# Performance work log

Measured on AMD Instinct MI355X. Metric: run time of the kernel, lower is better.

Reference implementation:

```python
import jax, jax.numpy as jnp
import numpy as np

N = 20000        # num_nodes
E = 320000       # num_edges
B = 2            # batch_size (query rows)
F = 64           # in_features == nrela_dim == out_features
R = 32           # num_relations
NEG_SLOPE = 0.2  # LeakyReLU alpha
RATIO = 0.5      # fixed ratio (ratio-given branch of forward)
ITERS = 4
LN_EPS = 1e-5


def setup_inputs() -> dict:
    key = jax.random.key(0)
    ks = jax.random.split(key, 12)
    return {
        "edge_index": jax.random.randint(ks[0], (2, E), 0, N),
        "r_index": jax.random.randint(ks[1], (E,), 0, R),
        "boudnary_input": jax.random.normal(ks[2], (N, B, F), dtype=jnp.float32),
        "query_input": jax.random.normal(ks[3], (B, F), dtype=jnp.float32),
        # relation_linear: in_features -> nrela_dim * num_relations (torch [out,in] layout)
        "rel_w": 0.02 * jax.random.normal(ks[4], (R * F, F), dtype=jnp.float32),
        "rel_b": jnp.zeros((R * F,), dtype=jnp.float32),
        # layer_linear: 2*in_features -> out_features
        "layer_w": 0.02 * jax.random.normal(ks[5], (F, 2 * F), dtype=jnp.float32),
        "layer_b": jnp.zeros((F,), dtype=jnp.float32),
        # trans_readout_linear: in_features -> out_features
        "tr_w": 0.02 * jax.random.normal(ks[6], (F, F), dtype=jnp.float32),
        "tr_b": jnp.zeros((F,), dtype=jnp.float32),
        "W": 0.02 * jax.random.normal(ks[7], (B * F, F), dtype=jnp.float32),
        "a": 0.02 * jax.random.normal(ks[8], (4, F, 1), dtype=jnp.float32),
        "ln_g": jnp.ones((F,), dtype=jnp.float32),
        "ln_b": jnp.zeros((F,), dtype=jnp.float32),
    }


def _one_iter(x, i, edge_index, r_index, query, rel_w, rel_b, layer_w, layer_b,
              tr_w, tr_b, W, a, ln_g, ln_b):
    src, dst = edge_index[0], edge_index[1]
    node_in = x[src]                                           # [E, B, F] gather
    rel = (query @ rel_w.T + rel_b).reshape(R, B, F)           # [R, B, F]
    edge_in = rel[r_index]                                     # [E, B, F]
    msg = node_in + edge_in                                    # [E, B, F]
    edge_h = msg.reshape(E, B * F) @ W                         # [E, F]
    alpha = jax.nn.leaky_relu(jnp.squeeze(edge_h @ a[i], -1), NEG_SLOPE)  # [E]
    # sparse softmax grouped by source node
    m = jax.ops.segment_max(alpha, src, num_segments=N)
    ex = jnp.exp(alpha - m[src])
    denom = jax.ops.segment_sum(ex, src, num_segments=N)
    alpha = ex / (denom[src] + 1e-16)
    # top-k mask over all edges
    k = int(E * RATIO)
    _, idx = jax.lax.top_k(alpha, k)
    mask = jnp.zeros((E,), dtype=bool).at[idx].set(True)
    alpha = jnp.where(mask, alpha, 0.0)
    # path_message: scatter-add of weighted messages by dst; the concatenated
    # self-loop part (ones * boundary scattered by arange) is exactly + x
    update = jax.ops.segment_sum(alpha[:, None, None] * msg, dst, num_segments=N) + x
    readout = jnp.mean(x, axis=0)                              # [B, F]
    out = jnp.concatenate([x, update], axis=-1) @ layer_w.T + layer_b  # [N, B, F]
    out = out + (readout @ tr_w.T + tr_b)                      # broadcast [B, F]
    mu = out.mean(-1, keepdims=True)
    var = out.var(-1, keepdims=True)
    out = (out - mu) / jnp.sqrt(var + LN_EPS) * ln_g + ln_b
    return jax.nn.elu(out)


def reference(edge_index, r_index, boudnary_input, query_input, rel_w, rel_b,
              layer_w, layer_b, tr_w, tr_b, W, a, ln_g, ln_b):
    x = boudnary_input
    for i in range(ITERS):  # ratio-given branch: iter_layer = 0..3
        h = _one_iter(x, i, edge_index, r_index, query_input, rel_w, rel_b,
                      layer_w, layer_b, tr_w, tr_b, W, a, ln_g, ln_b)
        x = h + x
    return x
```

## Files before the change

### kernel.cpp

```cpp
#include <hip/hip_runtime.h>
#include <stdint.h>

#define NN 20000
#define EE 320000
#define FF 64
#define ROW 128
#define KTOP 160000
#define NEG_SLOPE 0.2f
#define LN_EPS 1e-5f
#define H16BINS 16384
#define HBASE (120 << 11)
#define CCAP 16384
#define ASTR 136

typedef __attribute__((ext_vector_type(8))) short short8;
typedef __attribute__((ext_vector_type(4))) float f32x4;

__device__ __forceinline__ unsigned int bin_of(unsigned int u) {
  int b = (int)(u >> 12) - HBASE;
  b = b < 0 ? 0 : (b > (H16BINS - 1) ? (H16BINS - 1) : b);
  return (unsigned int)b;
}

__device__ __forceinline__ unsigned int f2bf(float v) {
  unsigned int u = __float_as_uint(v);
  return (u + 0x7FFFu + ((u >> 16) & 1u)) >> 16;
}

__device__ __forceinline__ unsigned long long pack4bf(float4 v) {
  unsigned long long a = (unsigned long long)f2bf(v.x);
  a |= (unsigned long long)f2bf(v.y) << 16;
  a |= (unsigned long long)f2bf(v.z) << 32;
  a |= (unsigned long long)f2bf(v.w) << 48;
  return a;
}

__global__ void precompute_kernel(const float* __restrict__ query,
                                  const float* __restrict__ rel_w,
                                  const float* __restrict__ rel_b,
                                  const float* __restrict__ W,
                                  const float* __restrict__ a,
                                  float* __restrict__ relflat,
                                  float* __restrict__ wa4) {
  int t = blockIdx.x * blockDim.x + threadIdx.x;
  if (t < 4096) {
    int bq = t >> 11, c = t & 2047;
    const float* q = query + bq * FF;
    const float* w = rel_w + (size_t)c * FF;
    float s = rel_b[c];
#pragma unroll
    for (int f = 0; f < FF; f++) s += q[f] * w[f];
    relflat[t] = s;
  }
  if (t < 512) {
    int i = t >> 7, j = t & 127;
    const float* av = a + i * FF;
    const float* w = W + (size_t)j * FF;
    float s = 0.f;
#pragma unroll
    for (int f = 0; f < FF; f++) s += w[f] * av[f];
    wa4[t] = s;
  }
}

__global__ void degcnt_kernel(const int* __restrict__ esrc, const int* __restrict__ edst,
                              unsigned int* __restrict__ deg_s, unsigned int* __restrict__ deg_d) {
  int e = blockIdx.x * blockDim.x + threadIdx.x;
  if (e < EE) {
    atomicAdd(deg_s + esrc[e], 1u);
    atomicAdd(deg_d + edst[e], 1u);
  }
}

__global__ void scan_kernel(const unsigned int* __restrict__ deg,
                            unsigned int* __restrict__ rowptr,
                            unsigned int* __restrict__ rowfill) {
  __shared__ unsigned int sh[1024];
  int t = threadIdx.x;
  const int PER = 20;
  unsigned int loc[PER];
  unsigned int sum = 0;
  int base = t * PER;
#pragma unroll
  for (int i = 0; i < PER; i++) {
    int n = base + i;
    unsigned int d = (n < NN) ? deg[n] : 0u;
    loc[i] = sum;
    sum += d;
  }
  sh[t] = sum;
  __syncthreads();
  for (int o = 1; o < 1024; o <<= 1) {
    unsigned int v = (t >= o) ? sh[t - o] : 0u;
    __syncthreads();
    sh[t] += v;
    __syncthreads();
  }
  unsigned int excl = sh[t] - sum;
#pragma unroll
  for (int i = 0; i < PER; i++) {
    int n = base + i;
    if (n < NN) {
      unsigned int rp = excl + loc[i];
      rowptr[n] = rp;
      rowfill[n] = rp;
    }
  }
  if (t == 1023) rowptr[NN] = EE;
}

__global__ void fill_kernel(const int* __restrict__ esrc, const int* __restrict__ edst,
                            const int* __restrict__ rix,
                            unsigned int* __restrict__ rowfill_s, unsigned int* __restrict__ rowfill_d,
                            unsigned int* __restrict__ cspack_s, int* __restrict__ csre_d) {
  int e = blockIdx.x * blockDim.x + threadIdx.x;
  if (e < EE) {
    unsigned int r = (unsigned int)rix[e];
    unsigned int ss = atomicAdd(rowfill_s + esrc[e], 1u);
    cspack_s[ss] = (unsigned int)e | (r << 19);
    unsigned int sd = atomicAdd(rowfill_d + edst[e], 1u);
    csre_d[sd] = e;
  }
}

__global__ void gatherd_kernel(const int* __restrict__ csre_d, const int* __restrict__ esrc,
                               const int* __restrict__ rix, unsigned int* __restrict__ packed_d,
                               unsigned int* __restrict__ pos_d) {
  int p = blockIdx.x * blockDim.x + threadIdx.x;
  if (p < EE) {
    int e = csre_d[p];
    packed_d[p] = (unsigned int)esrc[e] | ((unsigned int)rix[e] << 20);
    pos_d[e] = (unsigned int)p;
  }
}

__global__ void repack_kernel(unsigned int* __restrict__ cspack_s,
                              const unsigned int* __restrict__ pos_d) {
  int i = blockIdx.x * blockDim.x + threadIdx.x;
  if (i < EE) {
    unsigned int cs = cspack_s[i];
    cspack_s[i] = pos_d[cs & 0x7FFFFu] | (cs & 0xFFF80000u);
  }
}

__global__ void readout_kernel(const float* __restrict__ x, float* __restrict__ racc) {
  int j = threadIdx.x;
  float acc = 0.f;
  for (int n = blockIdx.x; n < NN; n += gridDim.x) acc += x[(size_t)n * ROW + j];
  atomicAdd(racc + j, acc);
}

__global__ void nodewa_kernel(const float* __restrict__ x, const float* __restrict__ wa,
                              float* __restrict__ nodewa) {
  int wave = threadIdx.x >> 6, lane = threadIdx.x & 63;
  float w0 = wa[lane], w1 = wa[64 + lane];
  for (int n = blockIdx.x * 4 + wave; n < NN; n += gridDim.x * 4) {
    float s = x[(size_t)n * ROW + lane] * w0 + x[(size_t)n * ROW + 64 + lane] * w1;
#pragma unroll
    for (int off = 32; off > 0; off >>= 1) s += __shfl_xor(s, off, 64);
    if (lane == 0) nodewa[n] = s;
  }
}

__global__ void trt_kernel(const float* __restrict__ racc_cur, const float* __restrict__ tr_w,
                           const float* __restrict__ tr_b, const float* __restrict__ layer_b,
                           float* __restrict__ trt_glob) {
  int t = threadIdx.x;
  int b = t >> 6, f = t & 63;
  const float invN = 1.0f / (float)NN;
  float s = tr_b[f] + layer_b[f];
  const float* rr = racc_cur + b * 64;
  const float* tw = tr_w + f * 64;
#pragma unroll 16
  for (int g = 0; g < 64; g++) s += rr[g] * invN * tw[g];
  trt_glob[t] = s;
}

__global__ __launch_bounds__(256) void alpha_csr_kernel(
    const unsigned int* __restrict__ rowptr_s, const unsigned int* __restrict__ cspack_s,
    const float* __restrict__ nodewa, const float* __restrict__ relflat,
    const float* __restrict__ wa, float* __restrict__ alpha_d,
    unsigned int* __restrict__ hist16, unsigned int* __restrict__ state) {
  __shared__ float relwa_sh[32];
  __shared__ unsigned int h16[H16BINS];
  int t = threadIdx.x;
  for (int i = t; i < H16BINS; i += 256) h16[i] = 0u;
  if (t < 32) {
    float s = 0.f;
    const float4* rf = (const float4*)(relflat + t * ROW);
    const float4* wf = (const float4*)wa;
#pragma unroll 8
    for (int j = 0; j < 32; j++) {
      float4 r4 = rf[j], w4 = wf[j];
      s += r4.x * w4.x + r4.y * w4.y + r4.z * w4.z + r4.w * w4.w;
    }
    relwa_sh[t] = s;
  }
  if (blockIdx.x == 0 && t == 255) { state[0] = 0u; state[1] = KTOP; }
  __syncthreads();
  int n = blockIdx.x * 256 + t;
  if (n < NN) {
    unsigned int p0 = rowptr_s[n], p1 = rowptr_s[n + 1];
    float nw = nodewa[n];
    float denom = 0.f;
    for (unsigned int p = p0; p < p1; p++) {
      unsigned int cs = cspack_s[p];
      float v = nw + relwa_sh[cs >> 19];
      v = v > 0.f ? v : NEG_SLOPE * v;
      denom += expf(v);
    }
    float inv = 1.0f / denom;
    for (unsigned int p = p0; p < p1; p++) {
      unsigned int cs = cspack_s[p];
      float v = nw + relwa_sh[cs >> 19];
      v = v > 0.f ? v : NEG_SLOPE * v;
      float av = expf(v) * inv;
      alpha_d[cs & 0x7FFFFu] = av;
      atomicAdd(&h16[bin_of(__float_as_uint(av))], 1u);
    }
  }
  __syncthreads();
  for (int i = t; i < H16BINS; i += 256) {
    unsigned int c = h16[i];
    if (c) atomicAdd(hist16 + i, c);
  }
}

__global__ void sel16_kernel(unsigned int* __restrict__ state, unsigned int* __restrict__ hist16) {
  __shared__ unsigned int sh[1024];
  int t = threadIdx.x;
  unsigned int s = 0;
  const unsigned int* hp = hist16 + t * (H16BINS / 1024);
#pragma unroll
  for (int i = 0; i < H16BINS / 1024; i++) s += hp[i];
  sh[t] = s;
  __syncthreads();
  for (int o = 1; o < 1024; o <<= 1) {
    unsigned int v = (t >= o) ? sh[t - o] : 0u;
    __syncthreads();
    sh[t] += v;
    __syncthreads();
  }
  unsigned int incl = sh[t];
  unsigned int total = sh[1023];
  unsigned int krem = state[1];
  unsigned int cumAbove = total - incl;
  if (t == 0) state[5] = 0u;
  if (cumAbove < krem && cumAbove + s >= krem) {
    unsigned int cum = cumAbove;
    for (int b = H16BINS / 1024 - 1; b >= 0; b--) {
      unsigned int c = hist16[t * (H16BINS / 1024) + b];
      if (cum + c >= krem) {
        state[0] = (unsigned int)(t * (H16BINS / 1024) + b);
        state[1] = krem - cum;
        break;
      }
      cum += c;
    }
  }
  for (int i = 0; i < H16BINS / 1024; i++) hist16[t * (H16BINS / 1024) + i] = 0u;
}

__global__ void cand_kernel(const float* __restrict__ alpha_d, unsigned int* __restrict__ state,
                            int* __restrict__ cand_p) {
  __shared__ int lbuf[256];
  __shared__ unsigned int lcnt;
  __shared__ unsigned int gbase;
  int t = threadIdx.x;
  if (t == 0) lcnt = 0u;
  __syncthreads();
  int p = blockIdx.x * 256 + t;
  if (p < EE) {
    unsigned int u = __float_as_uint(alpha_d[p]);
    if (bin_of(u) == state[0]) {
      unsigned int idx = atomicAdd(&lcnt, 1u);
      lbuf[idx] = p;
    }
  }
  __syncthreads();
  if (t == 0 && lcnt) gbase = atomicAdd(state + 5, lcnt);
  __syncthreads();
  if (t < (int)lcnt) {
    unsigned int pos = gbase + t;
    if (pos < CCAP) cand_p[pos] = lbuf[t];
  }
}

__global__ void final_kernel(float* __restrict__ alpha_d, const int* __restrict__ csre_d,
                             const int* __restrict__ cand_p, unsigned int* __restrict__ state) {
  __shared__ unsigned int hlow[4096];
  __shared__ unsigned int psum[256];
  __shared__ int tiebuf[2048];
  __shared__ unsigned int tcnt;
  __shared__ unsigned int sT, sNeed;
  int t = threadIdx.x;
  unsigned int cnt = state[5];
  if (cnt > CCAP) cnt = CCAP;
  unsigned int krem = state[1];
  for (int i = t; i < 4096; i += 256) hlow[i] = 0u;
  if (t == 0) { tcnt = 0u; sT = 0u; sNeed = 0xFFFFFFFFu; }
  __syncthreads();
  for (unsigned int i = t; i < cnt; i += 256)
    atomicAdd(&hlow[__float_as_uint(alpha_d[cand_p[i]]) & 0xFFFu], 1u);
  __syncthreads();
  unsigned int s = 0;
#pragma unroll
  for (int i = 0; i < 16; i++) s += hlow[t * 16 + i];
  psum[t] = s;
  __syncthreads();
  for (int o = 1; o < 256; o <<= 1) {
    unsigned int v = (t >= o) ? psum[t - o] : 0u;
    __syncthreads();
    psum[t] += v;
    __syncthreads();
  }
  unsigned int total = psum[255];
  unsigned int above_chunk = total - psum[t];
  if (above_chunk < krem && above_chunk + s >= krem) {
    unsigned int cum = above_chunk;
    for (int b = 15; b >= 0; b--) {
      unsigned int c = hlow[t * 16 + b];
      if (cum + c >= krem) {
        sT = ((state[0] + (unsigned int)HBASE) << 12) | (unsigned int)(t * 16 + b);
        sNeed = krem - cum;
        break;
      }
      cum += c;
    }
  }
  __syncthreads();
  unsigned int T = sT, need = sNeed;
  if (t == 0) { state[2] = T; state[3] = need; }
  for (unsigned int i = t; i < cnt; i += 256) {
    int p = cand_p[i];
    if (__float_as_uint(alpha_d[p]) == T) {
      unsigned int idx = atomicAdd(&tcnt, 1u);
      if (idx < 2048) tiebuf[idx] = p;
    }
  }
  __syncthreads();
  unsigned int tc = tcnt;
  if (tc > 2048) tc = 2048;
  if (tc > need) {
    for (unsigned int i = t; i < tc; i += 256) {
      int p = tiebuf[i];
      int e_i = csre_d[p];
      unsigned int rank = 0;
      for (unsigned int j = 0; j < tc; j++) rank += (csre_d[tiebuf[j]] < e_i) ? 1u : 0u;
      if (rank >= need) alpha_d[p] = 0.f;
    }
  }
}

__global__ __launch_bounds__(256) void update_kernel(const unsigned int* __restrict__ rowptr_d,
                                                     const unsigned int* __restrict__ packed_d,
                                                     const float* __restrict__ alpha_d,
                                                     const unsigned int* __restrict__ state,
                                                     const float* __restrict__ x,
                                                     const float* __restrict__ relflat,
                                                     float* __restrict__ upd,
                                                     float* __restrict__ racc_next) {
  __shared__ float relf[32 * 132];
  int t = threadIdx.x;
  if (blockIdx.x == 0 && t < 128) racc_next[t] = 0.f;
#pragma unroll
  for (int i = 0; i < 4; i++) {
    int q = t + i * 256;
    int r = q >> 5, kq = q & 31;
    float4 v = ((const float4*)relflat)[q];
    *(float4*)(relf + r * 132 + kq * 4) = v;
  }
  __syncthreads();
  unsigned int T = state[2];
  int wave = t >> 6, lane = t & 63;
  int g = lane >> 4, l = lane & 15;
  int n = blockIdx.x * 4 + wave;
  if (n >= NN) return;
  unsigned int p0 = rowptr_d[n], p1 = rowptr_d[n + 1];
  float4 A0 = {0.f, 0.f, 0.f, 0.f}, A1 = {0.f, 0.f, 0.f, 0.f};
  for (unsigned int base = p0 + g; base < p1; base += 4) {
    float w = alpha_d[base];
    if (__float_as_uint(w) < T) continue;
    unsigned int up = packed_d[base];
    unsigned int src = up & 0xFFFFFu;
    unsigned int r = up >> 20;
    const float* xr = x + (size_t)src * ROW + l * 8;
    const float* rr = relf + r * 132 + l * 8;
    float4 xv0 = *(const float4*)xr;
    float4 xv1 = *(const float4*)(xr + 4);
    float4 rv0 = *(const float4*)rr;
    float4 rv1 = *(const float4*)(rr + 4);
    A0.x += w * (xv0.x + rv0.x); A0.y += w * (xv0.y + rv0.y);
    A0.z += w * (xv0.z + rv0.z); A0.w += w * (xv0.w + rv0.w);
    A1.x += w * (xv1.x + rv1.x); A1.y += w * (xv1.y + rv1.y);
    A1.z += w * (xv1.z + rv1.z); A1.w += w * (xv1.w + rv1.w);
  }
#pragma unroll
  for (int off = 16; off <= 32; off <<= 1) {
    A0.x += __shfl_xor(A0.x, off, 64); A0.y += __shfl_xor(A0.y, off, 64);
    A0.z += __shfl_xor(A0.z, off, 64); A0.w += __shfl_xor(A0.w, off, 64);
    A1.x += __shfl_xor(A1.x, off, 64); A1.y += __shfl_xor(A1.y, off, 64);
    A1.z += __shfl_xor(A1.z, off, 64); A1.w += __shfl_xor(A1.w, off, 64);
  }
  if (g == 0) {
    const float* xn = x + (size_t)n * ROW + l * 8;
    float4 xs0 = *(const float4*)xn;
    float4 xs1 = *(const float4*)(xn + 4);
    float4 o0 = {A0.x + xs0.x, A0.y + xs0.y, A0.z + xs0.z, A0.w + xs0.w};
    float4 o1 = {A1.x + xs1.x, A1.y + xs1.y, A1.z + xs1.z, A1.w + xs1.w};
    float* on = upd + (size_t)n * ROW + l * 8;
    *(float4*)on = o0;
    *(float4*)(on + 4) = o1;
  }
}

__global__ __launch_bounds__(256) void node_mfma_kernel(const float* __restrict__ upd,
                                                        const float* __restrict__ layer_w,
                                                        const float* __restrict__ trt_glob,
                                                        const float* __restrict__ ln_g,
                                                        const float* __restrict__ ln_b,
                                                        float* __restrict__ x,
                                                        const float* __restrict__ wa_next,
                                                        float* __restrict__ nodewa,
                                                        float* __restrict__ racc_next) {
  __shared__ unsigned short Asb[64 * ASTR];
  __shared__ unsigned short Wsb[64 * ASTR];
  __shared__ float trt_sh[128];
  __shared__ float racc_sh[128];
  int t = threadIdx.x;
  int n0 = blockIdx.x * 32;
  if (t < 128) { trt_sh[t] = trt_glob[t]; racc_sh[t] = 0.f; }
#pragma unroll
  for (int i = 0; i < 4; i++) {
    int v = t + i * 256;
    int m = ((v >> 5) << 1) + ((v & 31) >> 4);
    int k = (v & 15) * 4;
    float4 xv = ((const float4*)x)[n0 * 32 + v];
    *(unsigned long long*)(Asb + m * ASTR + k) = pack4bf(xv);
    float4 uv = ((const float4*)upd)[n0 * 32 + v];
    *(unsigned long long*)(Asb + m * ASTR + 64 + k) = pack4bf(uv);
  }
#pragma unroll
  for (int i = 0; i < 8; i++) {
    int Q = t + i * 256;
    int f = Q >> 5, c4 = Q & 31;
    float4 wv = ((const float4*)layer_w)[Q];
    *(unsigned long long*)(Wsb + f * ASTR + c4 * 4) = pack4bf(wv);
  }
  __syncthreads();
  int lane = t & 63, mt = t >> 6;
  int l15 = lane & 15, q = lane >> 4;
  const unsigned short* arow = Asb + (mt * 16 + l15) * ASTR + q * 8;
  f32x4 acc[4] = {{0.f, 0.f, 0.f, 0.f}, {0.f, 0.f, 0.f, 0.f},
                  {0.f, 0.f, 0.f, 0.f}, {0.f, 0.f, 0.f, 0.f}};
#pragma unroll
  for (int ks = 0; ks < 4; ks++) {
    short8 a = *(const short8*)(arow + ks * 32);
#pragma unroll
    for (int nt = 0; nt < 4; nt++) {
      short8 b = *(const short8*)(Wsb + (nt * 16 + l15) * ASTR + ks * 32 + q * 8);
      acc[nt] = __builtin_amdgcn_mfma_f32_16x16x32_bf16(a, b, acc[nt], 0, 0, 0);
    }
  }
  float g_[4], bta[4], wn0[4], wn1[4], tr0[4], tr1[4];
#pragma unroll
  for (int nt = 0; nt < 4; nt++) {
    int f = nt * 16 + l15;
    g_[nt] = ln_g[f]; bta[nt] = ln_b[f];
    wn0[nt] = wa_next[f]; wn1[nt] = wa_next[64 + f];
    tr0[nt] = trt_sh[f]; tr1[nt] = trt_sh[64 + f];
  }
  const float invF = 1.0f / (float)FF;
  float y[4][4];
#pragma unroll
  for (int r = 0; r < 4; r++) {
    int b = r & 1;
    float o[4];
    float s = 0.f, qq = 0.f;
#pragma unroll
    for (int nt = 0; nt < 4; nt++) {
      float v = acc[nt][r] + (b ? tr1[nt] : tr0[nt]);
      o[nt] = v; s += v; qq += v * v;
    }
#pragma unroll
    for (int off = 1; off < 16; off <<= 1) {
      s += __shfl_xor(s, off, 64);
      qq += __shfl_xor(qq, off, 64);
    }
    float mu = s * invF;
    float var = qq * invF - mu * mu;
    float rstd = 1.0f / sqrtf(var + LN_EPS);
    int nl = mt * 8 + q * 2 + (r >> 1);
    size_t base = (size_t)(n0 + nl) * ROW + b * 64 + l15;
#pragma unroll
    for (int nt = 0; nt < 4; nt++) {
      float xo = x[base + nt * 16];
      float on = (o[nt] - mu) * rstd * g_[nt] + bta[nt];
      float h = on > 0.f ? on : expm1f(on);
      float yy = h + xo;
      y[r][nt] = yy;
      x[base + nt * 16] = yy;
    }
  }
#pragma unroll
  for (int b = 0; b < 2; b++) {
#pragma unroll
    for (int nt = 0; nt < 4; nt++) {
      atomicAdd(&racc_sh[b * 64 + nt * 16 + l15], y[b][nt] + y[b + 2][nt]);
    }
  }
#pragma unroll
  for (int rp = 0; rp < 2; rp++) {
    float nw = 0.f;
#pragma unroll
    for (int nt = 0; nt < 4; nt++)
      nw += y[2 * rp][nt] * wn0[nt] + y[2 * rp + 1][nt] * wn1[nt];
#pragma unroll
    for (int off = 1; off < 16; off <<= 1) nw += __shfl_xor(nw, off, 64);
    if (l15 == 0) nodewa[n0 + mt * 8 + q * 2 + rp] = nw;
  }
  __syncthreads();
  if (t < 128) atomicAdd(racc_next + t, racc_sh[t]);
}

extern "C" void kernel_launch(void* const* d_in, const int* in_sizes, int n_in,
                              void* d_out, int out_size, void* d_ws, size_t ws_size,
                              hipStream_t stream) {
  const int* ei = (const int*)d_in[0];
  const int* esrc = ei;
  const int* edst = ei + EE;
  const int* rix = (const int*)d_in[1];
  const float* boundary = (const float*)d_in[2];
  const float* query = (const float*)d_in[3];
  const float* rel_w = (const float*)d_in[4];
  const float* rel_b = (const float*)d_in[5];
  const float* layer_w = (const float*)d_in[6];
  const float* layer_b = (const float*)d_in[7];
  const float* tr_w = (const float*)d_in[8];
  const float* tr_b = (const float*)d_in[9];
  const float* Wm = (const float*)d_in[10];
  const float* av = (const float*)d_in[11];
  const float* ln_g = (const float*)d_in[12];
  const float* ln_b = (const float*)d_in[13];
  float* x = (float*)d_out;

  char* ws = (char*)d_ws;
  size_t off = 0;
  auto allocf = [&](size_t n) -> float* {
    float* p = (float*)(ws + off);
    off += ((n * 4 + 255) / 256) * 256;
    return p;
  };
  auto allocu = [&](size_t n) -> unsigned int* {
    unsigned int* p = (unsigned int*)(ws + off);
    off += ((n * 4 + 255) / 256) * 256;
    return p;
  };
  float* relflat = allocf(4096);
  float* wa4 = allocf(512);
  float* alpha_d = allocf(EE);
  float* upd = allocf((size_t)NN * ROW);
  float* racc0 = allocf(128);
  float* racc1 = allocf(128);
  float* trt_glob = allocf(128);
  float* nodewa = allocf(NN);
  unsigned int* hist16 = allocu(H16BINS);
  unsigned int* state = allocu(8);
  unsigned int* deg_s = allocu(NN);
  unsigned int* deg_d = allocu(NN);
  unsigned int* rowptr_s = allocu(NN + 1);
  unsigned int* rowptr_d = allocu(NN + 1);
  unsigned int* rowfill_s = allocu(NN);
  unsigned int* rowfill_d = allocu(NN);
  unsigned int* cspack_s = allocu(EE);
  int* csre_d = (int*)allocu(EE);
  unsigned int* packed_d = allocu(EE);
  unsigned int* pos_d = allocu(EE);
  int* cand_p = (int*)allocu(CCAP);
  float* rbuf[2] = {racc0, racc1};

  hipMemcpyAsync(x, boundary, (size_t)NN * ROW * 4, hipMemcpyDeviceToDevice, stream);
  hipMemsetAsync(deg_s, 0, NN * 4, stream);
  hipMemsetAsync(deg_d, 0, NN * 4, stream);
  hipMemsetAsync(racc0, 0, 128 * 4, stream);
  hipMemsetAsync(hist16, 0, H16BINS * 4, stream);
  precompute_kernel<<<16, 256, 0, stream>>>(query, rel_w, rel_b, Wm, av, relflat, wa4);

  degcnt_kernel<<<EE / 256, 256, 0, stream>>>(esrc, edst, deg_s, deg_d);
  scan_kernel<<<1, 1024, 0, stream>>>(deg_s, rowptr_s, rowfill_s);
  scan_kernel<<<1, 1024, 0, stream>>>(deg_d, rowptr_d, rowfill_d);
  fill_kernel<<<EE / 256, 256, 0, stream>>>(esrc, edst, rix, rowfill_s, rowfill_d, cspack_s, csre_d);
  gatherd_kernel<<<EE / 256, 256, 0, stream>>>(csre_d, esrc, rix, packed_d, pos_d);
  repack_kernel<<<EE / 256, 256, 0, stream>>>(cspack_s, pos_d);

  readout_kernel<<<256, 128, 0, stream>>>(x, racc0);
  nodewa_kernel<<<1250, 256, 0, stream>>>(x, wa4, nodewa);

  for (int it = 0; it < 4; it++) {
    float* rcur = rbuf[it & 1];
    float* rnxt = rbuf[(it + 1) & 1];
    const float* wa_it = wa4 + it * 128;
    const float* wa_nx = wa4 + (it < 3 ? it + 1 : 3) * 128;

    trt_kernel<<<1, 128, 0, stream>>>(rcur, tr_w, tr_b, layer_b, trt_glob);
    alpha_csr_kernel<<<(NN + 255) / 256, 256, 0, stream>>>(rowptr_s, cspack_s, nodewa,
                                                           relflat, wa_it, alpha_d, hist16, state);
    sel16_kernel<<<1, 1024, 0, stream>>>(state, hist16);
    cand_kernel<<<EE / 256, 256, 0, stream>>>(alpha_d, state, cand_p);
    final_kernel<<<1, 256, 0, stream>>>(alpha_d, csre_d, cand_p, state);

    update_kernel<<<5000, 256, 0, stream>>>(rowptr_d, packed_d, alpha_d, state, x, relflat,
                                            upd, rnxt);
    node_mfma_kernel<<<625, 256, 0, stream>>>(upd, layer_w, trt_glob, ln_g, ln_b, x,
                                              wa_nx, nodewa, rnxt);
  }
}
```

Before: 694.9 us.

## Fuse scatter-update, readout transform and node MFMA into one kernel

Merges update_kernel and node_mfma_kernel into a single fused kernel. The per-node weighted aggregation is now written straight into the shared-memory bf16 A tile, so the upd buffer no longer makes a global round trip. The trt computation is folded into the fused kernel and the racc zeroing moves to sel16, removing one tiny launch per iteration. x is ping-ponged between two buffers so neighbour gathers can read the old x while new rows are written. The cost is fewer blocks (625 of 256 threads, each wave walking 8 nodes serially) where there were 5000, which lowers the parallelism available to hide gather latency.

```diff
diff --git a/kernel.cpp b/kernel.cpp
--- a/kernel.cpp
+++ b/kernel.cpp
@@ -160,20 +160,6 @@
     for (int off = 32; off > 0; off >>= 1) s += __shfl_xor(s, off, 64);
     if (lane == 0) nodewa[n] = s;
   }
-}
-
-__global__ void trt_kernel(const float* __restrict__ racc_cur, const float* __restrict__ tr_w,
-                           const float* __restrict__ tr_b, const float* __restrict__ layer_b,
-                           float* __restrict__ trt_glob) {
-  int t = threadIdx.x;
-  int b = t >> 6, f = t & 63;
-  const float invN = 1.0f / (float)NN;
-  float s = tr_b[f] + layer_b[f];
-  const float* rr = racc_cur + b * 64;
-  const float* tw = tr_w + f * 64;
-#pragma unroll 16
-  for (int g = 0; g < 64; g++) s += rr[g] * invN * tw[g];
-  trt_glob[t] = s;
 }
 
 __global__ __launch_bounds__(256) void alpha_csr_kernel(
@@ -226,9 +212,11 @@
   }
 }
 
-__global__ void sel16_kernel(unsigned int* __restrict__ state, unsigned int* __restrict__ hist16) {
+__global__ void sel16_kernel(unsigned int* __restrict__ state, unsigned int* __restrict__ hist16,
+                             float* __restrict__ racc_next) {
   __shared__ unsigned int sh[1024];
   int t = threadIdx.x;
+  if (t < 128) racc_next[t] = 0.f;
   unsigned int s = 0;
   const unsigned int* hp = hist16 + t * (H16BINS / 1024);
 #pragma unroll
@@ -352,93 +340,36 @@
   }
 }
 
-__global__ __launch_bounds__(256) void update_kernel(const unsigned int* __restrict__ rowptr_d,
-                                                     const unsigned int* __restrict__ packed_d,
-                                                     const float* __restrict__ alpha_d,
-                                                     const unsigned int* __restrict__ state,
-                                                     const float* __restrict__ x,
-                                                     const float* __restrict__ relflat,
-                                                     float* __restrict__ upd,
-                                                     float* __restrict__ racc_next) {
+__global__ __launch_bounds__(256) void fused_kernel(const unsigned int* __restrict__ rowptr_d,
+                                                    const unsigned int* __restrict__ packed_d,
+                                                    const float* __restrict__ alpha_d,
+                                                    const unsigned int* __restrict__ state,
+                                                    const float* __restrict__ x_cur,
+                                                    float* __restrict__ x_next,
+                                                    const float* __restrict__ relflat,
+                                                    const float* __restrict__ layer_w,
+                                                    const float* __restrict__ racc_cur,
+                                                    const float* __restrict__ tr_w,
+                                                    const float* __restrict__ tr_b,
+                                                    const float* __restrict__ layer_b,
+                                                    const float* __restrict__ ln_g,
+                                                    const float* __restrict__ ln_b,
+                                                    const float* __restrict__ wa_next,
+                                                    float* __restrict__ nodewa,
+                                                    float* __restrict__ racc_next) {
   __shared__ float relf[32 * 132];
-  int t = threadIdx.x;
-  if (blockIdx.x == 0 && t < 128) racc_next[t] = 0.f;
-#pragma unroll
-  for (int i = 0; i < 4; i++) {
-    int q = t + i * 256;
-    int r = q >> 5, kq = q & 31;
-    float4 v = ((const float4*)relflat)[q];
-    *(float4*)(relf + r * 132 + kq * 4) = v;
-  }
-  __syncthreads();
-  unsigned int T = state[2];
-  int wave = t >> 6, lane = t & 63;
-  int g = lane >> 4, l = lane & 15;
-  int n = blockIdx.x * 4 + wave;
-  if (n >= NN) return;
-  unsigned int p0 = rowptr_d[n], p1 = rowptr_d[n + 1];
-  float4 A0 = {0.f, 0.f, 0.f, 0.f}, A1 = {0.f, 0.f, 0.f, 0.f};
-  for (unsigned int base = p0 + g; base < p1; base += 4) {
-    float w = alpha_d[base];
-    if (__float_as_uint(w) < T) continue;
-    unsigned int up = packed_d[base];
-    unsigned int src = up & 0xFFFFFu;
-    unsigned int r = up >> 20;
-    const float* xr = x + (size_t)src * ROW + l * 8;
-    const float* rr = relf + r * 132 + l * 8;
-    float4 xv0 = *(const float4*)xr;
-    float4 xv1 = *(const float4*)(xr + 4);
-    float4 rv0 = *(const float4*)rr;
-    float4 rv1 = *(const float4*)(rr + 4);
-    A0.x += w * (xv0.x + rv0.x); A0.y += w * (xv0.y + rv0.y);
-    A0.z += w * (xv0.z + rv0.z); A0.w += w * (xv0.w + rv0.w);
-    A1.x += w * (xv1.x + rv1.x); A1.y += w * (xv1.y + rv1.y);
-    A1.z += w * (xv1.z + rv1.z); A1.w += w * (xv1.w + rv1.w);
-  }
-#pragma unroll
-  for (int off = 16; off <= 32; off <<= 1) {
-    A0.x += __shfl_xor(A0.x, off, 64); A0.y += __shfl_xor(A0.y, off, 64);
-    A0.z += __shfl_xor(A0.z, off, 64); A0.w += __shfl_xor(A0.w, off, 64);
-    A1.x += __shfl_xor(A1.x, off, 64); A1.y += __shfl_xor(A1.y, off, 64);
-    A1.z += __shfl_xor(A1.z, off, 64); A1.w += __shfl_xor(A1.w, off, 64);
-  }
-  if (g == 0) {
-    const float* xn = x + (size_t)n * ROW + l * 8;
-    float4 xs0 = *(const float4*)xn;
-    float4 xs1 = *(const float4*)(xn + 4);
-    float4 o0 = {A0.x + xs0.x, A0.y + xs0.y, A0.z + xs0.z, A0.w + xs0.w};
-    float4 o1 = {A1.x + xs1.x, A1.y + xs1.y, A1.z + xs1.z, A1.w + xs1.w};
-    float* on = upd + (size_t)n * ROW + l * 8;
-    *(float4*)on = o0;
-    *(float4*)(on + 4) = o1;
-  }
-}
-
-__global__ __launch_bounds__(256) void node_mfma_kernel(const float* __restrict__ upd,
-                                                        const float* __restrict__ layer_w,
-                                                        const float* __restrict__ trt_glob,
-                                                        const float* __restrict__ ln_g,
-                                                        const float* __restrict__ ln_b,
-                                                        float* __restrict__ x,
-                                                        const float* __restrict__ wa_next,
-                                                        float* __restrict__ nodewa,
-                                                        float* __restrict__ racc_next) {
   __shared__ unsigned short Asb[64 * ASTR];
   __shared__ unsigned short Wsb[64 * ASTR];
   __shared__ float trt_sh[128];
   __shared__ float racc_sh[128];
   int t = threadIdx.x;
   int n0 = blockIdx.x * 32;
-  if (t < 128) { trt_sh[t] = trt_glob[t]; racc_sh[t] = 0.f; }
 #pragma unroll
   for (int i = 0; i < 4; i++) {
-    int v = t + i * 256;
-    int m = ((v >> 5) << 1) + ((v & 31) >> 4);
-    int k = (v & 15) * 4;
-    float4 xv = ((const float4*)x)[n0 * 32 + v];
-    *(unsigned long long*)(Asb + m * ASTR + k) = pack4bf(xv);
-    float4 uv = ((const float4*)upd)[n0 * 32 + v];
-    *(unsigned long long*)(Asb + m * ASTR + 64 + k) = pack4bf(uv);
+    int q = t + i * 256;
+    int r = q >> 5, kq = q & 31;
+    float4 v = ((const float4*)relflat)[q];
+    *(float4*)(relf + r * 132 + kq * 4) = v;
   }
 #pragma unroll
   for (int i = 0; i < 8; i++) {
@@ -447,9 +378,67 @@
     float4 wv = ((const float4*)layer_w)[Q];
     *(unsigned long long*)(Wsb + f * ASTR + c4 * 4) = pack4bf(wv);
   }
-  __syncthreads();
+  if (t < 128) {
+    int b = t >> 6, f = t & 63;
+    const float invN = 1.0f / (float)NN;
+    float s = tr_b[f] + layer_b[f];
+    const float* rr = racc_cur + b * 64;
+    const float* tw = tr_w + f * 64;
+#pragma unroll 16
+    for (int gg = 0; gg < 64; gg++) s += rr[gg] * invN * tw[gg];
+    trt_sh[t] = s;
+    racc_sh[t] = 0.f;
+  }
+  __syncthreads();
+
+  unsigned int T = state[2];
   int lane = t & 63, mt = t >> 6;
-  int l15 = lane & 15, q = lane >> 4;
+  int g = lane >> 4, l = lane & 15;
+  for (int i = 0; i < 8; i++) {
+    int nl = mt * 8 + i;
+    int n = n0 + nl;
+    unsigned int p0 = rowptr_d[n], p1 = rowptr_d[n + 1];
+    float4 A0 = {0.f, 0.f, 0.f, 0.f}, A1 = {0.f, 0.f, 0.f, 0.f};
+    for (unsigned int base = p0 + g; base < p1; base += 4) {
+      float w = alpha_d[base];
+      if (__float_as_uint(w) < T) continue;
+      unsigned int up = packed_d[base];
+      unsigned int src = up & 0xFFFFFu;
+      unsigned int r = up >> 20;
+      const float* xr = x_cur + (size_t)src * ROW + l * 8;
+      const float* rr = relf + r * 132 + l * 8;
+      float4 xv0 = *(const float4*)xr;
+      float4 xv1 = *(const float4*)(xr + 4);
+      float4 rv0 = *(const float4*)rr;
+      float4 rv1 = *(const float4*)(rr + 4);
+      A0.x += w * (xv0.x + rv0.x); A0.y += w * (xv0.y + rv0.y);
+      A0.z += w * (xv0.z + rv0.z); A0.w += w * (xv0.w + rv0.w);
+      A1.x += w * (xv1.x + rv1.x); A1.y += w * (xv1.y + rv1.y);
+      A1.z += w * (xv1.z + rv1.z); A1.w += w * (xv1.w + rv1.w);
+    }
+#pragma unroll
+    for (int off = 16; off <= 32; off <<= 1) {
+      A0.x += __shfl_xor(A0.x, off, 64); A0.y += __shfl_xor(A0.y, off, 64);
+      A0.z += __shfl_xor(A0.z, off, 64); A0.w += __shfl_xor(A0.w, off, 64);
+      A1.x += __shfl_xor(A1.x, off, 64); A1.y += __shfl_xor(A1.y, off, 64);
+      A1.z += __shfl_xor(A1.z, off, 64); A1.w += __shfl_xor(A1.w, off, 64);
+    }
+    if (g == 0) {
+      const float* xn = x_cur + (size_t)n * ROW + l * 8;
+      float4 xs0 = *(const float4*)xn;
+      float4 xs1 = *(const float4*)(xn + 4);
+      float4 u0 = {A0.x + xs0.x, A0.y + xs0.y, A0.z + xs0.z, A0.w + xs0.w};
+      float4 u1 = {A1.x + xs1.x, A1.y + xs1.y, A1.z + xs1.z, A1.w + xs1.w};
+      int m = nl * 2 + (l >> 3);
+      int f8 = (l & 7) * 8;
+      unsigned short* arow = Asb + m * ASTR;
+      *(unsigned long long*)(arow + f8) = pack4bf(xs0);
+      *(unsigned long long*)(arow + f8 + 4) = pack4bf(xs1);
+      *(unsigned long long*)(arow + 64 + f8) = pack4bf(u0);
+      *(unsigned long long*)(arow + 64 + f8 + 4) = pack4bf(u1);
+    }
+  }
+  int l15 = l, q = g;
   const unsigned short* arow = Asb + (mt * 16 + l15) * ASTR + q * 8;
   f32x4 acc[4] = {{0.f, 0.f, 0.f, 0.f}, {0.f, 0.f, 0.f, 0.f},
                   {0.f, 0.f, 0.f, 0.f}, {0.f, 0.f, 0.f, 0.f}};
@@ -494,12 +483,12 @@
     size_t base = (size_t)(n0 + nl) * ROW + b * 64 + l15;
 #pragma unroll
     for (int nt = 0; nt < 4; nt++) {
-      float xo = x[base + nt * 16];
+      float xo = x_cur[base + nt * 16];
       float on = (o[nt] - mu) * rstd * g_[nt] + bta[nt];
       float h = on > 0.f ? on : expm1f(on);
       float yy = h + xo;
       y[r][nt] = yy;
-      x[base + nt * 16] = yy;
+      x_next[base + nt * 16] = yy;
     }
   }
 #pragma unroll
@@ -559,10 +548,9 @@
   float* relflat = allocf(4096);
   float* wa4 = allocf(512);
   float* alpha_d = allocf(EE);
-  float* upd = allocf((size_t)NN * ROW);
+  float* xbuf = allocf((size_t)NN * ROW);
   float* racc0 = allocf(128);
   float* racc1 = allocf(128);
-  float* trt_glob = allocf(128);
   float* nodewa = allocf(NN);
   unsigned int* hist16 = allocu(H16BINS);
   unsigned int* state = allocu(8);
@@ -601,17 +589,18 @@
     float* rnxt = rbuf[(it + 1) & 1];
     const float* wa_it = wa4 + it * 128;
     const float* wa_nx = wa4 + (it < 3 ? it + 1 : 3) * 128;
-
-    trt_kernel<<<1, 128, 0, stream>>>(rcur, tr_w, tr_b, layer_b, trt_glob);
+    float* x_cur = (it & 1) ? xbuf : x;
+    float* x_nxt = (it & 1) ? x : xbuf;
+
     alpha_csr_kernel<<<(NN + 255) / 256, 256, 0, stream>>>(rowptr_s, cspack_s, nodewa,
                                                            relflat, wa_it, alpha_d, hist16, state);
-    sel16_kernel<<<1, 1024, 0, stream>>>(state, hist16);
+    sel16_kernel<<<1, 1024, 0, stream>>>(state, hist16, rnxt);
     cand_kernel<<<EE / 256, 256, 0, stream>>>(alpha_d, state, cand_p);
     final_kernel<<<1, 256, 0, stream>>>(alpha_d, csre_d, cand_p, state);
 
-    update_kernel<<<5000, 256, 0, stream>>>(rowptr_d, packed_d, alpha_d, state, x, relflat,
-                                            upd, rnxt);
-    node_mfma_kernel<<<625, 256, 0, stream>>>(upd, layer_w, trt_glob, ln_g, ln_b, x,
-                                              wa_nx, nodewa, rnxt);
-  }
-}
+    fused_kernel<<<625, 256, 0, stream>>>(rowptr_d, packed_d, alpha_d, state,
+                                          x_cur, x_nxt, relflat, layer_w,
+                                          rcur, tr_w, tr_b, layer_b, ln_g, ln_b,
+                                          wa_nx, nodewa, rnxt);
+  }
+}
```

New measurement: 711.0 us. +2.3%, slower.
